# Performance work log

Measured on AMD Instinct MI355X. Metric: run time of the kernel, lower is better.

## Reference

```python
import jax, jax.numpy as jnp
import numpy as np

IN_FEATURES = 1024
N_CLASSES = 50257
CUTOFFS = [4000, 20000, 50257]  # user cutoffs + [n_classes]
HEAD_SIZE = CUTOFFS[0] + 2      # shortlist + 2 cluster logits
HSZ = [IN_FEATURES // 2, IN_FEATURES // 4]  # div_value=2.0 -> 512, 256
N = 2048


def setup_inputs() -> dict:
    key = jax.random.key(0)
    ks = jax.random.split(key, 8)
    s = 0.02
    return {
        'inp': jax.random.normal(ks[0], (N, IN_FEATURES), dtype=jnp.float32),
        'tgt': jax.random.randint(ks[1], (N,), 0, N_CLASSES, dtype=jnp.int64),
        'head_w': jax.random.normal(ks[2], (HEAD_SIZE, IN_FEATURES), dtype=jnp.float32) * s,
        't0_w1': jax.random.normal(ks[3], (HSZ[0], IN_FEATURES), dtype=jnp.float32) * s,
        't0_w2': jax.random.normal(ks[4], (CUTOFFS[1] - CUTOFFS[0], HSZ[0]), dtype=jnp.float32) * s,
        't1_w1': jax.random.normal(ks[5], (HSZ[1], IN_FEATURES), dtype=jnp.float32) * s,
        't1_w2': jax.random.normal(ks[6], (CUTOFFS[2] - CUTOFFS[1], HSZ[1]), dtype=jnp.float32) * s,
    }


def _cluster_logprob(inp, w1, w2, rel, mask):
    # two-stage projection: [N,d] -> [N,h] -> [N,osz], then per-row log-softmax
    # gathered at the relative target column. Masked rows contribute 0.
    logits = (inp @ w1.T) @ w2.T                       # [N, osz]
    lse = jax.scipy.special.logsumexp(logits, axis=1)  # [N]
    rel_c = jnp.clip(rel, 0, logits.shape[1] - 1)
    tgt_logit = jnp.take_along_axis(logits, rel_c[:, None], axis=1)[:, 0]
    return jnp.where(mask, tgt_logit - lse, jnp.zeros_like(lse))


def reference(inp, tgt, head_w, t0_w1, t0_w2, t1_w1, t1_w2):
    c0, c1 = CUTOFFS[0], CUTOFFS[1]
    in0 = tgt < c0
    in1 = (tgt >= c0) & (tgt < c1)
    in2 = tgt >= c1

    # head: shortlist targets gather their own column; tail targets gather
    # their cluster's logit column (c0 + cluster_index - 1)
    head_logits = inp @ head_w.T                      # [N, HEAD_SIZE]
    head_lp = jax.nn.log_softmax(head_logits, axis=1)
    gather_inds = jnp.where(in0, tgt, jnp.where(in1, c0, c0 + 1))
    head_term = jnp.take_along_axis(head_lp, gather_inds[:, None], axis=1)[:, 0]

    out = head_term
    out = out + _cluster_logprob(inp, t0_w1, t0_w2, tgt - c0, in1)
    out = out + _cluster_logprob(inp, t1_w1, t1_w2, tgt - c1, in2)
    return -out  # per-sample NLL, shape [N]
```

## Files before the change

### kernel.cpp

```cpp
#include <hip/hip_runtime.h>
#include <cfloat>
#include <cmath>


#define N_ROWS 2048
#define K_IN   1024
#define HEAD_O 4002
#define CUT0   4000
#define CUT1   20000
#define T0_O   16000
#define T1_O   30257
#define H0     512
#define H1     256

#define HT   16
#define T0T  63
#define T1T  119

typedef __attribute__((ext_vector_type(8))) __bf16 bf16x8;
typedef __attribute__((ext_vector_type(4))) float f32x4;
typedef unsigned short u16;

__device__ inline u16 f2bf_rne(float f) {
    unsigned u = __builtin_bit_cast(unsigned, f);
    u += 0x7FFFu + ((u >> 16) & 1u);
    return (u16)(u >> 16);
}
__device__ inline float bf2f(u16 b) {
    return __builtin_bit_cast(float, (unsigned)b << 16);
}

__device__ inline void gload_lds16(const u16* g, u16* l) {
    __builtin_amdgcn_global_load_lds(
        (const __attribute__((address_space(1))) void*)g,
        (__attribute__((address_space(3))) void*)l, 16, 0, 0);
}

__global__ __launch_bounds__(256)
void split_all(const float* __restrict__ s0, const float* __restrict__ s1,
               const float* __restrict__ s2, const float* __restrict__ s3,
               const float* __restrict__ s4, const float* __restrict__ s5,
               u16* __restrict__ h0, u16* __restrict__ h1, u16* __restrict__ h2,
               u16* __restrict__ h3, u16* __restrict__ h4, u16* __restrict__ h5)
{
    constexpr int e0 = (N_ROWS * K_IN) / 4;
    constexpr int e1 = e0 + (HEAD_O * K_IN) / 4;
    constexpr int e2 = e1 + (H0 * K_IN) / 4;
    constexpr int e3 = e2 + (H1 * K_IN) / 4;
    constexpr int e4 = e3 + (T0_O * H0) / 4;
    constexpr int e5 = e4 + (T1_O * H1) / 4;
    for (int i = blockIdx.x * 256 + threadIdx.x; i < e5; i += gridDim.x * 256) {
        const float* src; u16* h; int off;
        if      (i < e0) { src = s0; h = h0; off = i; }
        else if (i < e1) { src = s1; h = h1; off = i - e0; }
        else if (i < e2) { src = s2; h = h2; off = i - e1; }
        else if (i < e3) { src = s3; h = h3; off = i - e2; }
        else if (i < e4) { src = s4; h = h4; off = i - e3; }
        else             { src = s5; h = h5; off = i - e4; }
        const float4 v = ((const float4*)src)[off];
        ushort4 hv;
        hv.x = f2bf_rne(v.x); hv.y = f2bf_rne(v.y);
        hv.z = f2bf_rne(v.z); hv.w = f2bf_rne(v.w);
        ((ushort4*)h)[off] = hv;
    }
}

__global__ __launch_bounds__(256)
void compact(const int* __restrict__ tgt, int* __restrict__ cnt,
             int* __restrict__ rowOf0, int* __restrict__ cidx0,
             int* __restrict__ rowOf1, int* __restrict__ cidx1)
{
    const int row = blockIdx.x * 256 + threadIdx.x;
    if (row >= N_ROWS) return;
    const int tg = tgt[row];
    if (tg >= CUT0 && tg < CUT1) {
        const int s = atomicAdd(&cnt[0], 1);
        rowOf0[s] = row; cidx0[row] = s;
    } else if (tg >= CUT1) {
        const int s = atomicAdd(&cnt[1], 1);
        rowOf1[s] = row; cidx1[row] = s;
    }
}

__device__ inline void map8(int bid, int T, int& panel, int& rowt)
{
    const int full = T & ~7;
    const int fb = full << 3;
    if (bid < fb) {
        panel = ((bid >> 6) << 3) + (bid & 7);
        rowt  = (bid >> 3) & 7;
    } else {
        const int l = bid - fb;
        panel = full + (l >> 3);
        rowt  = l & 7;
    }
}

template<bool LSE>
__device__ __forceinline__ void gemm256_core(
    u16* lds,
    const u16* __restrict__ A, const u16* __restrict__ B,
    int K, int O, int T, int bx, int by,
    const int* __restrict__ rowIdx,
    float* __restrict__ Pm, float* __restrict__ Ps,
    u16* __restrict__ Ch)
{
    const int t = threadIdx.x;
    const int lane = t & 63;
    const int w = t >> 6;
    const int row0 = by * 256, col0 = bx * 256;
    const int kg = lane >> 4, li = lane & 15;
    const int wr = w >> 2, wc = w & 3;

    const u16* gsrc[4];
    {
        const int slot = t & 3;
        const int rbase = t >> 2;
        #pragma unroll
        for (int i = 0; i < 4; ++i) {
            const int p = i >> 1, half = i & 1;
            const int rl = half * 128 + rbase;
            const int kd = (slot ^ ((rl >> 1) & 3)) * 8;
            const u16* base; int grow;
            if (p == 0) {
                grow = row0 + rl;
                if (rowIdx) grow = rowIdx[grow] & (N_ROWS - 1);
                base = A;
            } else {
                grow = col0 + rl; if (grow > O - 1) grow = O - 1;
                base = B;
            }
            gsrc[i] = base + (size_t)grow * K + kd;
        }
    }
    u16* ldsb = lds + t * 8;

    int aoff[8], boff[4];
    #pragma unroll
    for (int m = 0; m < 8; ++m) {
        const int ar = wr * 128 + m * 16 + li;
        aoff[m] = ar * 64 + ((kg ^ ((ar >> 1) & 3)) << 4);
    }
    #pragma unroll
    for (int n = 0; n < 4; ++n) {
        const int bc = wc * 64 + n * 16 + li;
        boff[n] = 16384 + bc * 64 + ((kg ^ ((bc >> 1) & 3)) << 4);
    }

    f32x4 acc[8][4];
    #pragma unroll
    for (int m = 0; m < 8; ++m)
        #pragma unroll
        for (int n = 0; n < 4; ++n) acc[m][n] = (f32x4){0.f, 0.f, 0.f, 0.f};

    const char* ldsc = (const char*)lds;
    const int nsteps = K >> 5;

    auto compute_step = [&](const char* bufc) {
        bf16x8 fb[4];
        #pragma unroll
        for (int n = 0; n < 4; ++n) fb[n] = *(const bf16x8*)(bufc + boff[n]);
        __builtin_amdgcn_s_setprio(1);
        #pragma unroll
        for (int m = 0; m < 8; ++m) {
            const bf16x8 fa = *(const bf16x8*)(bufc + aoff[m]);
            #pragma unroll
            for (int n = 0; n < 4; ++n)
                acc[m][n] = __builtin_amdgcn_mfma_f32_16x16x32_bf16(fa, fb[n], acc[m][n], 0, 0, 0);
        }
        __builtin_amdgcn_s_setprio(0);
    };

    #pragma unroll
    for (int i = 0; i < 4; ++i)
        gload_lds16(gsrc[i], ldsb + (i >> 1) * 8192 + (i & 1) * 4096);

    for (int ks = 0; ks < nsteps - 1; ++ks) {
        const int cur = ks & 1;
        {
            const int nxt = (cur ^ 1) * 16384;
            const int kof = (ks + 1) * 32;
            #pragma unroll
            for (int i = 0; i < 4; ++i)
                gload_lds16(gsrc[i] + kof, ldsb + nxt + (i >> 1) * 8192 + (i & 1) * 4096);
        }
        asm volatile("s_waitcnt vmcnt(4)" ::: "memory");
        __builtin_amdgcn_s_barrier();
        compute_step(ldsc + cur * 32768);
        asm volatile("" ::: "memory");
        __builtin_amdgcn_s_barrier();
    }
    asm volatile("s_waitcnt vmcnt(0)" ::: "memory");
    __builtin_amdgcn_s_barrier();
    compute_step(ldsc + ((nsteps - 1) & 1) * 32768);
    asm volatile("" ::: "memory");
    __builtin_amdgcn_s_barrier();

    if (LSE) {
        float* pmS = (float*)lds;
        float* psS = (float*)lds + 1024;
        #pragma unroll
        for (int m = 0; m < 8; ++m) {
            #pragma unroll
            for (int r = 0; r < 4; ++r) {
                const int row_l = wr * 128 + m * 16 + kg * 4 + r;
                float mx = -FLT_MAX, sm = 0.f;
                float vv[4]; bool ok[4];
                #pragma unroll
                for (int n = 0; n < 4; ++n) {
                    const int c = col0 + wc * 64 + n * 16 + li;
                    ok[n] = (c < O);
                    vv[n] = acc[m][n][r];
                    if (ok[n]) mx = fmaxf(mx, vv[n]);
                }
                #pragma unroll
                for (int n = 0; n < 4; ++n)
                    if (ok[n]) sm += __expf(vv[n] - mx);
                #pragma unroll
                for (int off = 1; off < 16; off <<= 1) {
                    const float mo = __shfl_xor(mx, off);
                    const float so = __shfl_xor(sm, off);
                    const float M2 = fmaxf(mx, mo);
                    sm = sm * __expf(mx - M2) + so * __expf(mo - M2);
                    mx = M2;
                }
                if (li == 0) { pmS[row_l * 4 + wc] = mx; psS[row_l * 4 + wc] = sm; }
            }
        }
        __syncthreads();
        if (t < 256) {
            float M = -FLT_MAX, S = 0.f;
            #pragma unroll
            for (int q = 0; q < 4; ++q) {
                const float mq = pmS[t * 4 + q], sq = psS[t * 4 + q];
                const float M2 = fmaxf(M, mq);
                S = S * __expf(M - M2) + sq * __expf(mq - M2);
                M = M2;
            }
            Pm[(size_t)(row0 + t) * T + bx] = M;
            Ps[(size_t)(row0 + t) * T + bx] = S;
        }
    } else {
        #pragma unroll
        for (int m = 0; m < 8; ++m)
            #pragma unroll
            for (int n = 0; n < 4; ++n)
                #pragma unroll
                for (int r = 0; r < 4; ++r) {
                    const int row = row0 + wr * 128 + m * 16 + kg * 4 + r;
                    const int col = col0 + wc * 64 + n * 16 + li;
                    Ch[(size_t)row * O + col] = f2bf_rne(acc[m][n][r]);
                }
    }
}

__global__ __launch_bounds__(512)
void projhead(const u16* __restrict__ ih,   const u16* __restrict__ hwh,
              const u16* __restrict__ w10h, const u16* __restrict__ w11h,
              const int* __restrict__ cnt,
              const int* __restrict__ rowOf0, const int* __restrict__ rowOf1,
              float* __restrict__ hPm, float* __restrict__ hPs,
              u16* __restrict__ t0hh, u16* __restrict__ t1hh)
{
    __shared__ u16 lds[32768];
    const int bid = blockIdx.x;
    int bx, by;
    if (bid < HT * 8) {
        map8(bid, HT, bx, by);
        gemm256_core<true>(lds, ih, hwh, K_IN, HEAD_O, HT, bx, by,
                           nullptr, hPm, hPs, nullptr);
    } else if (bid < HT * 8 + 16) {
        const int b = bid - HT * 8;
        bx = b >> 3; by = b & 7;
        if (by * 256 >= cnt[0]) return;
        gemm256_core<false>(lds, ih, w10h, K_IN, H0, 2, bx, by,
                            rowOf0, nullptr, nullptr, t0hh);
    } else {
        const int b = bid - HT * 8 - 16;
        by = b & 7;
        if (by * 256 >= cnt[1]) return;
        gemm256_core<false>(lds, ih, w11h, K_IN, H1, 1, 0, by,
                            rowOf1, nullptr, nullptr, t1hh);
    }
}

__global__ __launch_bounds__(512)
void lse_tails(const u16* __restrict__ t0hh, const u16* __restrict__ w20h,
               const u16* __restrict__ t1hh, const u16* __restrict__ w21h,
               const int* __restrict__ cnt,
               float* __restrict__ p0m, float* __restrict__ p0s,
               float* __restrict__ p1m, float* __restrict__ p1s)
{
    __shared__ u16 lds[32768];
    const int bid = blockIdx.x;
    int bx, by;
    if (bid < T0T * 8) {
        map8(bid, T0T, bx, by);
        if (by * 256 >= cnt[0]) return;
        gemm256_core<true>(lds, t0hh, w20h, H0, T0_O, T0T, bx, by,
                           nullptr, p0m, p0s, nullptr);
    } else {
        map8(bid - T0T * 8, T1T, bx, by);
        if (by * 256 >= cnt[1]) return;
        gemm256_core<true>(lds, t1hh, w21h, H1, T1_O, T1T, bx, by,
                           nullptr, p1m, p1s, nullptr);
    }
}

__device__ inline float block_sum(float v, float* sm)
{
#pragma unroll
    for (int off = 32; off > 0; off >>= 1) v += __shfl_xor(v, off);
    __syncthreads();
    if ((threadIdx.x & 63) == 0) sm[threadIdx.x >> 6] = v;
    __syncthreads();
    return sm[0] + sm[1] + sm[2] + sm[3];
}

__device__ inline void block_lse(float& m, float& s, float* smm, float* sms)
{
#pragma unroll
    for (int off = 32; off > 0; off >>= 1) {
        const float mo = __shfl_xor(m, off);
        const float so = __shfl_xor(s, off);
        const float M2 = fmaxf(m, mo);
        s = s * __expf(m - M2) + so * __expf(mo - M2);
        m = M2;
    }
    __syncthreads();
    if ((threadIdx.x & 63) == 0) { smm[threadIdx.x >> 6] = m; sms[threadIdx.x >> 6] = s; }
    __syncthreads();
    const float M2 = fmaxf(fmaxf(smm[0], smm[1]), fmaxf(smm[2], smm[3]));
    const float S  = sms[0] * __expf(smm[0] - M2) + sms[1] * __expf(smm[1] - M2)
                   + sms[2] * __expf(smm[2] - M2) + sms[3] * __expf(smm[3] - M2);
    m = M2; s = S;
}

__device__ inline void local_lse(const float* __restrict__ Pm,
                                 const float* __restrict__ Ps,
                                 int T, float& m, float& s)
{
    m = -FLT_MAX; s = 0.f;
    for (int i = threadIdx.x; i < T; i += 256) {
        const float mi = Pm[i], si = Ps[i];
        const float M2 = fmaxf(m, mi);
        s = s * __expf(m - M2) + si * __expf(mi - M2);
        m = M2;
    }
}

__global__ __launch_bounds__(256)
void finalize(const float* __restrict__ inp, const int* __restrict__ tgt,
              const float* __restrict__ head_w,
              const int* __restrict__ cidx0, const int* __restrict__ cidx1,
              const u16* __restrict__ t0hh, const u16* __restrict__ t1hh,
              const float* __restrict__ hPm, const float* __restrict__ hPs, int hT,
              const float* __restrict__ p0m, const float* __restrict__ p0s, int T0,
              const float* __restrict__ p1m, const float* __restrict__ p1s, int T1,
              const float* __restrict__ t0_w2, const float* __restrict__ t1_w2,
              float* __restrict__ out)
{
    __shared__ float sm[4], ss[4];
    const int row = blockIdx.x, t = threadIdx.x;
    const int tg = tgt[row];
    const bool in1 = (tg >= CUT0) && (tg < CUT1);
    const bool in2 = (tg >= CUT1);
    const int g = (tg < CUT0) ? tg : (in1 ? CUT0 : CUT0 + 1);
    const int c0 = in1 ? cidx0[row] : 0;
    const int c1 = in2 ? cidx1[row] : 0;

    float d;
    {
        const float4 a = *(const float4*)(inp + (size_t)row * K_IN + t * 4);
        const float4 b = *(const float4*)(head_w + (size_t)g * K_IN + t * 4);
        d = a.x * b.x + a.y * b.y + a.z * b.z + a.w * b.w;
    }
    const float dot_h = block_sum(d, sm);

    int r0 = tg - CUT0; r0 = r0 < 0 ? 0 : (r0 > T0_O - 1 ? T0_O - 1 : r0);
    d = 0.f;
    if (t < 128) {
        const ushort4 a = *(const ushort4*)(t0hh + (size_t)c0 * H0 + t * 4);
        const float4  b = *(const float4*)(t0_w2 + (size_t)r0 * H0 + t * 4);
        d = bf2f(a.x) * b.x + bf2f(a.y) * b.y + bf2f(a.z) * b.z + bf2f(a.w) * b.w;
    }
    const float dot0 = block_sum(d, sm);

    int r1 = tg - CUT1; r1 = r1 < 0 ? 0 : (r1 > T1_O - 1 ? T1_O - 1 : r1);
    d = 0.f;
    if (t < 64) {
        const ushort4 a = *(const ushort4*)(t1hh + (size_t)c1 * H1 + t * 4);
        const float4  b = *(const float4*)(t1_w2 + (size_t)r1 * H1 + t * 4);
        d = bf2f(a.x) * b.x + bf2f(a.y) * b.y + bf2f(a.z) * b.z + bf2f(a.w) * b.w;
    }
    const float dot1 = block_sum(d, sm);

    float m, s;
    local_lse(hPm + (size_t)row * hT, hPs + (size_t)row * hT, hT, m, s);
    block_lse(m, s, sm, ss);
    const float lse_h = m + logf(s);

    local_lse(p0m + (size_t)c0 * T0, p0s + (size_t)c0 * T0, T0, m, s);
    block_lse(m, s, sm, ss);
    const float lse_0 = m + logf(s);

    local_lse(p1m + (size_t)c1 * T1, p1s + (size_t)c1 * T1, T1, m, s);
    block_lse(m, s, sm, ss);
    const float lse_1 = m + logf(s);

    if (t == 0) {
        float res = dot_h - lse_h;
        if (in1) res += dot0 - lse_0;
        if (in2) res += dot1 - lse_1;
        out[row] = -res;
    }
}

extern "C" void kernel_launch(void* const* d_in, const int* in_sizes, int n_in,
                              void* d_out, int out_size, void* d_ws, size_t ws_size,
                              hipStream_t stream)
{
    const float* inp    = (const float*)d_in[0];
    const int*   tgt    = (const int*)  d_in[1];
    const float* head_w = (const float*)d_in[2];
    const float* t0_w1  = (const float*)d_in[3];
    const float* t0_w2  = (const float*)d_in[4];
    const float* t1_w1  = (const float*)d_in[5];
    const float* t1_w2  = (const float*)d_in[6];
    float* out = (float*)d_out;

    char* p = (char*)d_ws;
    #define ALLOC(name, type, count) \
        type* name = (type*)p; p += (((size_t)(count) * sizeof(type)) + 255) & ~(size_t)255;
    ALLOC(hPm,  float, (size_t)N_ROWS * HT)
    ALLOC(hPs,  float, (size_t)N_ROWS * HT)
    ALLOC(p0m,  float, (size_t)N_ROWS * T0T)
    ALLOC(p0s,  float, (size_t)N_ROWS * T0T)
    ALLOC(p1m,  float, (size_t)N_ROWS * T1T)
    ALLOC(p1s,  float, (size_t)N_ROWS * T1T)
    ALLOC(ih,   u16, (size_t)N_ROWS * K_IN)
    ALLOC(hwh,  u16, (size_t)HEAD_O * K_IN)
    ALLOC(w10h, u16, (size_t)H0 * K_IN)
    ALLOC(w11h, u16, (size_t)H1 * K_IN)
    ALLOC(w20h, u16, (size_t)T0_O * H0)
    ALLOC(w21h, u16, (size_t)T1_O * H1)
    ALLOC(t0hh, u16, (size_t)N_ROWS * H0)
    ALLOC(t1hh, u16, (size_t)N_ROWS * H1)
    ALLOC(cnt,    int, 2)
    ALLOC(rowOf0, int, N_ROWS)
    ALLOC(cidx0,  int, N_ROWS)
    ALLOC(rowOf1, int, N_ROWS)
    ALLOC(cidx1,  int, N_ROWS)
    #undef ALLOC

    hipMemsetAsync(cnt, 0, 2 * sizeof(int), stream);
    compact<<<dim3(N_ROWS / 256), dim3(256), 0, stream>>>(tgt, cnt, rowOf0, cidx0, rowOf1, cidx1);

    split_all<<<dim3(2048), dim3(256), 0, stream>>>(
        inp, head_w, t0_w1, t1_w1, t0_w2, t1_w2,
        ih, hwh, w10h, w11h, w20h, w21h);

    projhead<<<dim3(HT * 8 + 16 + 8), dim3(512), 0, stream>>>(
        ih, hwh, w10h, w11h, cnt, rowOf0, rowOf1, hPm, hPs, t0hh, t1hh);

    lse_tails<<<dim3(T0T * 8 + T1T * 8), dim3(512), 0, stream>>>(
        t0hh, w20h, t1hh, w21h, cnt, p0m, p0s, p1m, p1s);

    finalize<<<dim3(N_ROWS), dim3(256), 0, stream>>>(
        inp, tgt, head_w, cidx0, cidx1, t0hh, t1hh,
        hPm, hPs, HT, p0m, p0s, T0T, p1m, p1s, T1T, t0_w2, t1_w2, out);
}
```

Measured before the change: 305.3 us.

## Fuse compaction into split kernel, move head GEMM into tail LSE launch

Folds the target compaction into the bf16 conversion kernel as extra blocks, which removes one launch. The head GEMM+LSE moves from the projection kernel into the tail-LSE kernel, so the projection launch becomes a small 24-block kernel and the big launch holds all LSE tiles for better load balance. The per-row LSE reduction also becomes a two-pass max-then-sum shuffle reduction instead of an online merge, which cuts the exp calls. In exchange the tiny projection kernel leaves most of the GPU idle while it runs, and the second kernel's timing now depends on it.

```diff
diff --git a/kernel.cpp b/kernel.cpp
--- a/kernel.cpp
+++ b/kernel.cpp
@@ -37,19 +37,35 @@
 }
 
 __global__ __launch_bounds__(256)
-void split_all(const float* __restrict__ s0, const float* __restrict__ s1,
-               const float* __restrict__ s2, const float* __restrict__ s3,
-               const float* __restrict__ s4, const float* __restrict__ s5,
-               u16* __restrict__ h0, u16* __restrict__ h1, u16* __restrict__ h2,
-               u16* __restrict__ h3, u16* __restrict__ h4, u16* __restrict__ h5)
-{
+void split_compact(const float* __restrict__ s0, const float* __restrict__ s1,
+                   const float* __restrict__ s2, const float* __restrict__ s3,
+                   const float* __restrict__ s4, const float* __restrict__ s5,
+                   u16* __restrict__ h0, u16* __restrict__ h1, u16* __restrict__ h2,
+                   u16* __restrict__ h3, u16* __restrict__ h4, u16* __restrict__ h5,
+                   const int* __restrict__ tgt, int* __restrict__ cnt,
+                   int* __restrict__ rowOf0, int* __restrict__ cidx0,
+                   int* __restrict__ rowOf1, int* __restrict__ cidx1)
+{
+    if (blockIdx.x >= 2048) {
+        const int row = (blockIdx.x - 2048) * 256 + threadIdx.x;
+        if (row >= N_ROWS) return;
+        const int tg = tgt[row];
+        if (tg >= CUT0 && tg < CUT1) {
+            const int s = atomicAdd(&cnt[0], 1);
+            rowOf0[s] = row; cidx0[row] = s;
+        } else if (tg >= CUT1) {
+            const int s = atomicAdd(&cnt[1], 1);
+            rowOf1[s] = row; cidx1[row] = s;
+        }
+        return;
+    }
     constexpr int e0 = (N_ROWS * K_IN) / 4;
     constexpr int e1 = e0 + (HEAD_O * K_IN) / 4;
     constexpr int e2 = e1 + (H0 * K_IN) / 4;
     constexpr int e3 = e2 + (H1 * K_IN) / 4;
     constexpr int e4 = e3 + (T0_O * H0) / 4;
     constexpr int e5 = e4 + (T1_O * H1) / 4;
-    for (int i = blockIdx.x * 256 + threadIdx.x; i < e5; i += gridDim.x * 256) {
+    for (int i = blockIdx.x * 256 + threadIdx.x; i < e5; i += 2048 * 256) {
         const float* src; u16* h; int off;
         if      (i < e0) { src = s0; h = h0; off = i; }
         else if (i < e1) { src = s1; h = h1; off = i - e0; }
@@ -62,23 +78,6 @@
         hv.x = f2bf_rne(v.x); hv.y = f2bf_rne(v.y);
         hv.z = f2bf_rne(v.z); hv.w = f2bf_rne(v.w);
         ((ushort4*)h)[off] = hv;
-    }
-}
-
-__global__ __launch_bounds__(256)
-void compact(const int* __restrict__ tgt, int* __restrict__ cnt,
-             int* __restrict__ rowOf0, int* __restrict__ cidx0,
-             int* __restrict__ rowOf1, int* __restrict__ cidx1)
-{
-    const int row = blockIdx.x * 256 + threadIdx.x;
-    if (row >= N_ROWS) return;
-    const int tg = tgt[row];
-    if (tg >= CUT0 && tg < CUT1) {
-        const int s = atomicAdd(&cnt[0], 1);
-        rowOf0[s] = row; cidx0[row] = s;
-    } else if (tg >= CUT1) {
-        const int s = atomicAdd(&cnt[1], 1);
-        rowOf1[s] = row; cidx1[row] = s;
     }
 }
 
@@ -204,26 +203,21 @@
             #pragma unroll
             for (int r = 0; r < 4; ++r) {
                 const int row_l = wr * 128 + m * 16 + kg * 4 + r;
-                float mx = -FLT_MAX, sm = 0.f;
-                float vv[4]; bool ok[4];
+                float vv[4];
                 #pragma unroll
                 for (int n = 0; n < 4; ++n) {
                     const int c = col0 + wc * 64 + n * 16 + li;
-                    ok[n] = (c < O);
-                    vv[n] = acc[m][n][r];
-                    if (ok[n]) mx = fmaxf(mx, vv[n]);
+                    vv[n] = (c < O) ? acc[m][n][r] : -FLT_MAX;
                 }
+                float mx = fmaxf(fmaxf(vv[0], vv[1]), fmaxf(vv[2], vv[3]));
                 #pragma unroll
-                for (int n = 0; n < 4; ++n)
-                    if (ok[n]) sm += __expf(vv[n] - mx);
+                for (int off = 1; off < 16; off <<= 1)
+                    mx = fmaxf(mx, __shfl_xor(mx, off));
+                float sm = __expf(vv[0] - mx) + __expf(vv[1] - mx)
+                         + __expf(vv[2] - mx) + __expf(vv[3] - mx);
                 #pragma unroll
-                for (int off = 1; off < 16; off <<= 1) {
-                    const float mo = __shfl_xor(mx, off);
-                    const float so = __shfl_xor(sm, off);
-                    const float M2 = fmaxf(mx, mo);
-                    sm = sm * __expf(mx - M2) + so * __expf(mo - M2);
-                    mx = M2;
-                }
+                for (int off = 1; off < 16; off <<= 1)
+                    sm += __shfl_xor(sm, off);
                 if (li == 0) { pmS[row_l * 4 + wc] = mx; psS[row_l * 4 + wc] = sm; }
             }
         }
@@ -255,12 +249,35 @@
 }
 
 __global__ __launch_bounds__(512)
-void projhead(const u16* __restrict__ ih,   const u16* __restrict__ hwh,
-              const u16* __restrict__ w10h, const u16* __restrict__ w11h,
-              const int* __restrict__ cnt,
-              const int* __restrict__ rowOf0, const int* __restrict__ rowOf1,
-              float* __restrict__ hPm, float* __restrict__ hPs,
-              u16* __restrict__ t0hh, u16* __restrict__ t1hh)
+void proj(const u16* __restrict__ ih,
+          const u16* __restrict__ w10h, const u16* __restrict__ w11h,
+          const int* __restrict__ cnt,
+          const int* __restrict__ rowOf0, const int* __restrict__ rowOf1,
+          u16* __restrict__ t0hh, u16* __restrict__ t1hh)
+{
+    __shared__ u16 lds[32768];
+    const int bid = blockIdx.x;
+    if (bid < 16) {
+        const int bx = bid >> 3, by = bid & 7;
+        if (by * 256 >= cnt[0]) return;
+        gemm256_core<false>(lds, ih, w10h, K_IN, H0, 2, bx, by,
+                            rowOf0, nullptr, nullptr, t0hh);
+    } else {
+        const int by = (bid - 16) & 7;
+        if (by * 256 >= cnt[1]) return;
+        gemm256_core<false>(lds, ih, w11h, K_IN, H1, 1, 0, by,
+                            rowOf1, nullptr, nullptr, t1hh);
+    }
+}
+
+__global__ __launch_bounds__(512)
+void lse_all(const u16* __restrict__ ih,   const u16* __restrict__ hwh,
+             const u16* __restrict__ t0hh, const u16* __restrict__ w20h,
+             const u16* __restrict__ t1hh, const u16* __restrict__ w21h,
+             const int* __restrict__ cnt,
+             float* __restrict__ hPm, float* __restrict__ hPs,
+             float* __restrict__ p0m, float* __restrict__ p0s,
+             float* __restrict__ p1m, float* __restrict__ p1s)
 {
     __shared__ u16 lds[32768];
     const int bid = blockIdx.x;
@@ -269,38 +286,13 @@
         map8(bid, HT, bx, by);
         gemm256_core<true>(lds, ih, hwh, K_IN, HEAD_O, HT, bx, by,
                            nullptr, hPm, hPs, nullptr);
-    } else if (bid < HT * 8 + 16) {
-        const int b = bid - HT * 8;
-        bx = b >> 3; by = b & 7;
-        if (by * 256 >= cnt[0]) return;
-        gemm256_core<false>(lds, ih, w10h, K_IN, H0, 2, bx, by,
-                            rowOf0, nullptr, nullptr, t0hh);
-    } else {
-        const int b = bid - HT * 8 - 16;
-        by = b & 7;
-        if (by * 256 >= cnt[1]) return;
-        gemm256_core<false>(lds, ih, w11h, K_IN, H1, 1, 0, by,
-                            rowOf1, nullptr, nullptr, t1hh);
-    }
-}
-
-__global__ __launch_bounds__(512)
-void lse_tails(const u16* __restrict__ t0hh, const u16* __restrict__ w20h,
-               const u16* __restrict__ t1hh, const u16* __restrict__ w21h,
-               const int* __restrict__ cnt,
-               float* __restrict__ p0m, float* __restrict__ p0s,
-               float* __restrict__ p1m, float* __restrict__ p1s)
-{
-    __shared__ u16 lds[32768];
-    const int bid = blockIdx.x;
-    int bx, by;
-    if (bid < T0T * 8) {
-        map8(bid, T0T, bx, by);
+    } else if (bid < HT * 8 + T0T * 8) {
+        map8(bid - HT * 8, T0T, bx, by);
         if (by * 256 >= cnt[0]) return;
         gemm256_core<true>(lds, t0hh, w20h, H0, T0_O, T0T, bx, by,
                            nullptr, p0m, p0s, nullptr);
     } else {
-        map8(bid - T0T * 8, T1T, bx, by);
+        map8(bid - HT * 8 - T0T * 8, T1T, bx, by);
         if (by * 256 >= cnt[1]) return;
         gemm256_core<true>(lds, t1hh, w21h, H1, T1_O, T1T, bx, by,
                            nullptr, p1m, p1s, nullptr);
@@ -454,17 +446,18 @@
     #undef ALLOC
 
     hipMemsetAsync(cnt, 0, 2 * sizeof(int), stream);
-    compact<<<dim3(N_ROWS / 256), dim3(256), 0, stream>>>(tgt, cnt, rowOf0, cidx0, rowOf1, cidx1);
-
-    split_all<<<dim3(2048), dim3(256), 0, stream>>>(
+
+    split_compact<<<dim3(2048 + 8), dim3(256), 0, stream>>>(
         inp, head_w, t0_w1, t1_w1, t0_w2, t1_w2,
-        ih, hwh, w10h, w11h, w20h, w21h);
-
-    projhead<<<dim3(HT * 8 + 16 + 8), dim3(512), 0, stream>>>(
-        ih, hwh, w10h, w11h, cnt, rowOf0, rowOf1, hPm, hPs, t0hh, t1hh);
-
-    lse_tails<<<dim3(T0T * 8 + T1T * 8), dim3(512), 0, stream>>>(
-        t0hh, w20h, t1hh, w21h, cnt, p0m, p0s, p1m, p1s);
+        ih, hwh, w10h, w11h, w20h, w21h,
+        tgt, cnt, rowOf0, cidx0, rowOf1, cidx1);
+
+    proj<<<dim3(24), dim3(512), 0, stream>>>(
+        ih, w10h, w11h, cnt, rowOf0, rowOf1, t0hh, t1hh);
+
+    lse_all<<<dim3(HT * 8 + T0T * 8 + T1T * 8), dim3(512), 0, stream>>>(
+        ih, hwh, t0hh, w20h, t1hh, w21h, cnt,
+        hPm, hPs, p0m, p0s, p1m, p1s);
 
     finalize<<<dim3(N_ROWS), dim3(256), 0, stream>>>(
         inp, tgt, head_w, cidx0, cidx1, t0hh, t1hh,
```

After: 302.2 us. About the same (-1.0%).
